# Optimization experiments

Hardware: AMD Instinct MI355X
Metric: run time of the kernel (lower is better)

Reference implementation:

```python
import jax, jax.numpy as jnp
import numpy as np

B, T, D, HS = 8, 2048, 768, 64  # batch, seq, n_embd, head_size


def setup_inputs() -> dict:
    key = jax.random.key(0)
    kx, kq, kk, kv = jax.random.split(key, 4)
    scale = 1.0 / np.sqrt(D)
    return {
        "x": jax.random.normal(kx, (B, T, D), dtype=jnp.float32),
        "Wq": jax.random.normal(kq, (D, HS), dtype=jnp.float32) * scale,
        "Wk": jax.random.normal(kk, (D, HS), dtype=jnp.float32) * scale,
        "Wv": jax.random.normal(kv, (D, HS), dtype=jnp.float32) * scale,
    }


def reference(x, Wq, Wk, Wv):
    # q,k,v: [B,T,HS]
    q = jnp.einsum("btd,dh->bth", x, Wq)
    k = jnp.einsum("btd,dh->bth", x, Wk)
    v = jnp.einsum("btd,dh->bth", x, Wv)
    hs = k.shape[-1]
    # scaled scores: [B,T,T]
    wei = jnp.einsum("bth,bsh->bts", q, k) * (hs ** -0.5)
    # causal mask (lower-triangular keeps, upper -> -inf)
    causal = jnp.tril(jnp.ones((x.shape[1], x.shape[1]), dtype=bool))
    wei = jnp.where(causal[None, :, :], wei, -jnp.inf)
    wei = jax.nn.softmax(wei, axis=-1)
    return jnp.einsum("bts,bsh->bth", wei, v)
```

## Files before the change

### kernel.cpp

```cpp
#include <hip/hip_runtime.h>

typedef float  f32x4  __attribute__((ext_vector_type(4)));
typedef short  short8 __attribute__((ext_vector_type(8)));
typedef short  short4_ __attribute__((ext_vector_type(4)));

constexpr int Bb = 8, T = 2048, D = 768, HS = 64;
constexpr int BT = Bb * T;
constexpr int QT = T / 64;
constexpr int PSTRIDE = 64 * 64 + 128;

__device__ __forceinline__ short f2bf(float f) {
    unsigned u = __builtin_bit_cast(unsigned, f);
    unsigned r = (u + 0x7FFFu + ((u >> 16) & 1u)) >> 16;
    return (short)r;
}

__device__ __forceinline__ void gld_lds16(const short* g, short* l) {
    __builtin_amdgcn_global_load_lds(
        (const __attribute__((address_space(1))) unsigned int*)g,
        (__attribute__((address_space(3))) unsigned int*)l, 16, 0, 0);
}

__global__ __launch_bounds__(256) void wt_kernel(const float* __restrict__ Wq,
                                                 const float* __restrict__ Wk,
                                                 const float* __restrict__ Wv,
                                                 short* __restrict__ Wt) {
    int n = blockIdx.x;
    const float* W = (n < 64) ? Wq : (n < 128) ? Wk : Wv;
    int c = n & 63;
    for (int kk = threadIdx.x; kk < D; kk += 256)
        Wt[n * D + kk] = f2bf(W[kk * HS + c]);
}

__global__ __launch_bounds__(512) void qkv_proj(const float* __restrict__ x,
                                                const short* __restrict__ Wt,
                                                short* __restrict__ qws,
                                                short* __restrict__ kws,
                                                short* __restrict__ vtg) {
    __shared__ alignas(16) short xs[2][64 * 72];
    __shared__ alignas(16) short wtile[2][192 * 64];

    const int tid  = threadIdx.x;
    const int lane = tid & 63, w = tid >> 6;
    const int lo   = lane & 15, hi = lane >> 4;
    const int wr   = w >> 2, wc = w & 3;
    const int row0 = blockIdx.x * 64;
    const int b    = row0 >> 11, t0 = row0 & 2047;

    const int xr0 = tid >> 4, xsg = tid & 15;
    const float* xsrc0 = &x[(size_t)(row0 + xr0) * D + xsg * 4];
    const float* xsrc1 = &x[(size_t)(row0 + 32 + xr0) * D + xsg * 4];

    f32x4 acc[6];
#pragma unroll
    for (int j = 0; j < 6; j++) acc[j] = f32x4{0.f, 0.f, 0.f, 0.f};

#define STAGE(bb, kc)                                                          \
    {                                                                          \
        _Pragma("unroll")                                                      \
        for (int it = 0; it < 3; it++) {                                       \
            int ci = it * 512 + w * 64 + lane;                                 \
            int n = ci >> 3, seg = ci & 7;                                     \
            gld_lds16(&Wt[(size_t)n * D + (kc) * 64 + ((seg ^ (n & 7)) << 3)], \
                      &wtile[bb][(it * 512 + w * 64) * 8]);                    \
        }                                                                      \
        float4 f0 = *reinterpret_cast<const float4*>(xsrc0 + (kc) * 64);       \
        float4 f1 = *reinterpret_cast<const float4*>(xsrc1 + (kc) * 64);       \
        short4_ h0, h1;                                                        \
        h0[0] = f2bf(f0.x); h0[1] = f2bf(f0.y); h0[2] = f2bf(f0.z); h0[3] = f2bf(f0.w); \
        h1[0] = f2bf(f1.x); h1[1] = f2bf(f1.y); h1[2] = f2bf(f1.z); h1[3] = f2bf(f1.w); \
        *reinterpret_cast<short4_*>(&xs[bb][xr0 * 72 + xsg * 4]) = h0;         \
        *reinterpret_cast<short4_*>(&xs[bb][(32 + xr0) * 72 + xsg * 4]) = h1;  \
    }

    STAGE(0, 0);
    __syncthreads();

    for (int kc = 0; kc < 12; kc++) {
        const int bb = kc & 1;
        if (kc + 1 < 12) STAGE(bb ^ 1, kc + 1);

#pragma unroll
        for (int m = 0; m < 2; m++) {
            const int ar = (wr * 32 + m * 16 + lo) * 72;
            short8 a0 = *reinterpret_cast<const short8*>(&xs[bb][ar + hi * 8]);
            short8 a1 = *reinterpret_cast<const short8*>(&xs[bb][ar + 32 + hi * 8]);
#pragma unroll
            for (int j = 0; j < 3; j++) {
                const int row = wc * 48 + j * 16 + lo;
                const int rx  = (row & 7) << 3;
                short8 b0 = *reinterpret_cast<const short8*>(
                    &wtile[bb][row * 64 + ((hi << 3) ^ rx)]);
                short8 b1 = *reinterpret_cast<const short8*>(
                    &wtile[bb][row * 64 + (((hi + 4) << 3) ^ rx)]);
                acc[m * 3 + j] = __builtin_amdgcn_mfma_f32_16x16x32_bf16(a0, b0, acc[m * 3 + j], 0, 0, 0);
                acc[m * 3 + j] = __builtin_amdgcn_mfma_f32_16x16x32_bf16(a1, b1, acc[m * 3 + j], 0, 0, 0);
            }
        }
        __syncthreads();
    }
#undef STAGE

#pragma unroll
    for (int m = 0; m < 2; m++) {
        const int orow = row0 + wr * 32 + m * 16 + hi * 4;
#pragma unroll
        for (int j = 0; j < 3; j++) {
            const int cb = wc * 48 + j * 16;
            const f32x4 a = acc[m * 3 + j];
            if (cb < 64) {
#pragma unroll
                for (int r = 0; r < 4; r++)
                    qws[(size_t)(orow + r) * HS + cb + lo] = f2bf(a[r] * 0.125f);
            } else if (cb < 128) {
#pragma unroll
                for (int r = 0; r < 4; r++)
                    kws[(size_t)(orow + r) * HS + cb - 64 + lo] = f2bf(a[r]);
            } else {
                short4_ pv;
#pragma unroll
                for (int r = 0; r < 4; r++) pv[r] = f2bf(a[r]);
                *reinterpret_cast<short4_*>(
                    &vtg[((size_t)b * 64 + cb - 128 + lo) * T + t0 + wr * 32 + m * 16 + hi * 4]) = pv;
            }
        }
    }
}

__global__ __launch_bounds__(256, 4) void attn(const short* __restrict__ qg,
                                               const short* __restrict__ kg,
                                               const short* __restrict__ vtg,
                                               float* __restrict__ part, int S) {
    __shared__ short ks[2][64 * 64];
    __shared__ short vts[2][64 * 64];
    __shared__ short ps[4][16 * 64];

    const int tid  = threadIdx.x;
    const int lane = tid & 63, w = tid >> 6;
    const int lo   = lane & 15, hi = lane >> 4;
    const int bid  = blockIdx.x;
    const int per_b = QT * S;
    const int b    = bid / per_b;
    const int r2   = bid % per_b;
    const int qt   = 31 - (r2 / S);
    const int c    = r2 % S;
    const int nkt  = qt + 1;
    const int base = nkt / S, rem = nkt % S;
    const int niter = base + (c < rem ? 1 : 0);
    const int kt0   = c * base + (c < rem ? c : rem);
    float* pout = part + (size_t)((b * QT + qt) * S + c) * PSTRIDE;

    float m_ = -1e30f, l_ = 0.0f;
    f32x4 oacc[4];
#pragma unroll
    for (int i = 0; i < 4; i++) oacc[i] = f32x4{0.f, 0.f, 0.f, 0.f};

    if (niter > 0) {
        const int qrow = qt * 64 + w * 16 + lo;
        const size_t qbase = ((size_t)b * T + qrow) * HS;
        short8 qa0 = *reinterpret_cast<const short8*>(&qg[qbase + hi * 8]);
        short8 qa1 = *reinterpret_cast<const short8*>(&qg[qbase + 32 + hi * 8]);

        const int srow = tid >> 2, scs = tid & 3, r7 = srow & 7;
        const int w0 = srow * 64 + (((scs * 2)     ^ r7) << 3);
        const int w1 = srow * 64 + (((scs * 2 + 1) ^ r7) << 3);
        const size_t kgoff = (size_t)b * T * HS;
        const size_t vgoff = ((size_t)b * 64 + srow) * T;

        short8 ka, kb2, va, vb;
        {
            const short* kp = &kg[kgoff + (size_t)(kt0 * 64 + srow) * HS + scs * 16];
            ka = *reinterpret_cast<const short8*>(kp);
            kb2 = *reinterpret_cast<const short8*>(kp + 8);
            const short* vp = &vtg[vgoff + kt0 * 64 + scs * 16];
            va = *reinterpret_cast<const short8*>(vp);
            vb = *reinterpret_cast<const short8*>(vp + 8);
        }
        *reinterpret_cast<short8*>(&ks[0][w0])  = ka;
        *reinterpret_cast<short8*>(&ks[0][w1])  = kb2;
        *reinterpret_cast<short8*>(&vts[0][w0]) = va;
        *reinterpret_cast<short8*>(&vts[0][w1]) = vb;

        const int pswz = (lo & 7) << 3;
        int cur = 0;
        for (int i = 0; i < niter; i++) {
            const int kt = kt0 + i;
            if (i + 1 < niter) {
                const short* kp = &kg[kgoff + (size_t)((kt + 1) * 64 + srow) * HS + scs * 16];
                ka = *reinterpret_cast<const short8*>(kp);
                kb2 = *reinterpret_cast<const short8*>(kp + 8);
                const short* vp = &vtg[vgoff + (kt + 1) * 64 + scs * 16];
                va = *reinterpret_cast<const short8*>(vp);
                vb = *reinterpret_cast<const short8*>(vp + 8);
            }
            __syncthreads();

            f32x4 sacc[4];
#pragma unroll
            for (int nt = 0; nt < 4; nt++) sacc[nt] = f32x4{0.f, 0.f, 0.f, 0.f};
            __builtin_amdgcn_s_setprio(1);
#pragma unroll
            for (int nt = 0; nt < 4; nt++) {
                const int row = nt * 16 + lo, rr = row & 7;
                short8 b0 = *reinterpret_cast<const short8*>(
                    &ks[cur][row * 64 + ((hi ^ rr) << 3)]);
                short8 b1 = *reinterpret_cast<const short8*>(
                    &ks[cur][row * 64 + (((hi + 4) ^ rr) << 3)]);
                sacc[nt] = __builtin_amdgcn_mfma_f32_16x16x32_bf16(b0, qa0, sacc[nt], 0, 0, 0);
                sacc[nt] = __builtin_amdgcn_mfma_f32_16x16x32_bf16(b1, qa1, sacc[nt], 0, 0, 0);
            }
            __builtin_amdgcn_s_setprio(0);

            if (kt == qt) {
#pragma unroll
                for (int nt = 0; nt < 4; nt++)
#pragma unroll
                    for (int r = 0; r < 4; r++)
                        if (nt * 16 + hi * 4 + r > w * 16 + lo) sacc[nt][r] = -1e30f;
            }

            float tm = fmaxf(fmaxf(fmaxf(sacc[0][0], sacc[0][1]), fmaxf(sacc[0][2], sacc[0][3])),
                             fmaxf(fmaxf(sacc[1][0], sacc[1][1]), fmaxf(sacc[1][2], sacc[1][3])));
            tm = fmaxf(tm, fmaxf(fmaxf(fmaxf(sacc[2][0], sacc[2][1]), fmaxf(sacc[2][2], sacc[2][3])),
                                 fmaxf(fmaxf(sacc[3][0], sacc[3][1]), fmaxf(sacc[3][2], sacc[3][3]))));
            tm = fmaxf(tm, __shfl_xor(tm, 16));
            tm = fmaxf(tm, __shfl_xor(tm, 32));

            if (!__all(tm <= m_ + 8.0f)) {
                float mnew = fmaxf(m_, tm);
                float corr = __expf(m_ - mnew);
                l_ *= corr;
#pragma unroll
                for (int r = 0; r < 4; r++) {
                    float cr = __shfl(corr, (lane & 48) | (hi * 4 + r));
#pragma unroll
                    for (int nt = 0; nt < 4; nt++) oacc[nt][r] *= cr;
                }
                m_ = mnew;
            }

#pragma unroll
            for (int nt = 0; nt < 4; nt++)
#pragma unroll
                for (int r = 0; r < 4; r++) {
                    float p = __expf(sacc[nt][r] - m_);
                    l_ += p;
                    const int key = nt * 16 + hi * 4 + r;
                    ps[w][lo * 64 + (key ^ pswz)] = f2bf(p);
                }

            short8 pa0 = *reinterpret_cast<const short8*>(
                &ps[w][lo * 64 + ((hi << 3) ^ pswz)]);
            short8 pa1 = *reinterpret_cast<const short8*>(
                &ps[w][lo * 64 + (((hi + 4) << 3) ^ pswz)]);
            __builtin_amdgcn_s_setprio(1);
#pragma unroll
            for (int nt = 0; nt < 4; nt++) {
                const int row = nt * 16 + lo, rr = row & 7;
                short8 b0 = *reinterpret_cast<const short8*>(
                    &vts[cur][row * 64 + ((hi ^ rr) << 3)]);
                short8 b1 = *reinterpret_cast<const short8*>(
                    &vts[cur][row * 64 + (((hi + 4) ^ rr) << 3)]);
                oacc[nt] = __builtin_amdgcn_mfma_f32_16x16x32_bf16(pa0, b0, oacc[nt], 0, 0, 0);
                oacc[nt] = __builtin_amdgcn_mfma_f32_16x16x32_bf16(pa1, b1, oacc[nt], 0, 0, 0);
            }
            __builtin_amdgcn_s_setprio(0);

            if (i + 1 < niter) {
                *reinterpret_cast<short8*>(&ks[cur ^ 1][w0])  = ka;
                *reinterpret_cast<short8*>(&ks[cur ^ 1][w1])  = kb2;
                *reinterpret_cast<short8*>(&vts[cur ^ 1][w0]) = va;
                *reinterpret_cast<short8*>(&vts[cur ^ 1][w1]) = vb;
            }
            cur ^= 1;
        }
    }

    float lt = l_;
    lt += __shfl_xor(lt, 16);
    lt += __shfl_xor(lt, 32);

#pragma unroll
    for (int nt = 0; nt < 4; nt++)
#pragma unroll
        for (int r = 0; r < 4; r++)
            pout[(w * 16 + hi * 4 + r) * 64 + nt * 16 + lo] = oacc[nt][r];
    float mfor[4], lfor[4];
#pragma unroll
    for (int r = 0; r < 4; r++) {
        mfor[r] = __shfl(m_, (lane & 48) | (hi * 4 + r));
        lfor[r] = __shfl(lt, (lane & 48) | (hi * 4 + r));
    }
    if (lo == 0) {
#pragma unroll
        for (int r = 0; r < 4; r++) {
            const int row = w * 16 + hi * 4 + r;
            pout[4096 + row] = mfor[r];
            pout[4160 + row] = lfor[r];
        }
    }
}

__global__ __launch_bounds__(256) void combine(const float* __restrict__ part,
                                               float* __restrict__ out, int S) {
    const int bid = blockIdx.x;
    const int b = bid >> 5, qt = bid & 31;
    const float* p = part + (size_t)bid * S * PSTRIDE;
    const int row = threadIdx.x >> 2, cs = threadIdx.x & 3;

    float mv[4], lv[4], av[4];
    float M = -1e30f;
    for (int s = 0; s < S; s++) {
        mv[s] = p[(size_t)s * PSTRIDE + 4096 + row];
        lv[s] = p[(size_t)s * PSTRIDE + 4160 + row];
        M = fmaxf(M, mv[s]);
    }
    float den = 0.0f;
    for (int s = 0; s < S; s++) { av[s] = __expf(mv[s] - M); den += lv[s] * av[s]; }
    float inv = 1.0f / den;

    float* o = out + ((size_t)b * T + qt * 64 + row) * HS + cs * 16;
#pragma unroll
    for (int i = 0; i < 4; i++) {
        float4 res = make_float4(0.f, 0.f, 0.f, 0.f);
        for (int s = 0; s < S; s++) {
            float4 v = *reinterpret_cast<const float4*>(
                p + (size_t)s * PSTRIDE + row * 64 + cs * 16 + i * 4);
            res.x += v.x * av[s]; res.y += v.y * av[s];
            res.z += v.z * av[s]; res.w += v.w * av[s];
        }
        res.x *= inv; res.y *= inv; res.z *= inv; res.w *= inv;
        *reinterpret_cast<float4*>(o + i * 4) = res;
    }
}

extern "C" void kernel_launch(void* const* d_in, const int* in_sizes, int n_in,
                              void* d_out, int out_size, void* d_ws, size_t ws_size,
                              hipStream_t stream) {
    const float* x  = (const float*)d_in[0];
    const float* Wq = (const float*)d_in[1];
    const float* Wk = (const float*)d_in[2];
    const float* Wv = (const float*)d_in[3];
    float* out = (float*)d_out;

    short* ws   = (short*)d_ws;
    short* qws  = ws;
    short* kws  = qws + (size_t)BT * HS;
    short* vtws = kws + (size_t)BT * HS;
    short* Wt   = vtws + (size_t)BT * HS;
    float* part = (float*)(Wt + (size_t)192 * D);

    const size_t fixed = (size_t)3 * BT * HS * 2 + (size_t)192 * D * 2;
    int S = 4;
    while (S > 1 && fixed + (size_t)Bb * QT * S * PSTRIDE * 4 > ws_size) S >>= 1;

    wt_kernel<<<192, 256, 0, stream>>>(Wq, Wk, Wv, Wt);
    qkv_proj<<<BT / 64, 512, 0, stream>>>(x, Wt, qws, kws, vtws);
    attn<<<Bb * QT * S, 256, 0, stream>>>(qws, kws, vtws, part, S);
    combine<<<Bb * QT, 256, 0, stream>>>(part, out, S);
}
```

Baseline: 56.24 us.

## Triple-buffer QKV projection with async global-to-LDS loads for x and W

The QKV projection kernel now loads the fp32 x tile straight into LDS with global_load_lds, using an XOR swizzle. The bf16 conversion moves to fragment-load time, after the LDS read. Both the x and W tiles are triple-buffered with three stages prefetched. Manual vmcnt waits plus raw s_barrier replace __syncthreads, so loads can stay in flight across iterations. This should hide global-load latency and take the register round-trip for x off the load path. In exchange, LDS use is much larger, which may cut occupancy, and each x element is converted redundantly by the waves that share it.

```diff
diff --git a/kernel.cpp b/kernel.cpp
--- a/kernel.cpp
+++ b/kernel.cpp
@@ -15,7 +15,7 @@
     return (short)r;
 }
 
-__device__ __forceinline__ void gld_lds16(const short* g, short* l) {
+__device__ __forceinline__ void gld_lds16(const void* g, void* l) {
     __builtin_amdgcn_global_load_lds(
         (const __attribute__((address_space(1))) unsigned int*)g,
         (__attribute__((address_space(3))) unsigned int*)l, 16, 0, 0);
@@ -37,8 +37,8 @@
                                                 short* __restrict__ qws,
                                                 short* __restrict__ kws,
                                                 short* __restrict__ vtg) {
-    __shared__ alignas(16) short xs[2][64 * 72];
-    __shared__ alignas(16) short wtile[2][192 * 64];
+    __shared__ alignas(16) short wtile[3][192 * 64];
+    __shared__ alignas(16) float xls[3][64 * 64];
 
     const int tid  = threadIdx.x;
     const int lane = tid & 63, w = tid >> 6;
@@ -47,59 +47,86 @@
     const int row0 = blockIdx.x * 64;
     const int b    = row0 >> 11, t0 = row0 & 2047;
 
-    const int xr0 = tid >> 4, xsg = tid & 15;
-    const float* xsrc0 = &x[(size_t)(row0 + xr0) * D + xsg * 4];
-    const float* xsrc1 = &x[(size_t)(row0 + 32 + xr0) * D + xsg * 4];
-
     f32x4 acc[6];
 #pragma unroll
     for (int j = 0; j < 6; j++) acc[j] = f32x4{0.f, 0.f, 0.f, 0.f};
 
-#define STAGE(bb, kc)                                                          \
+#define STAGE_W(bufi, kc)                                                      \
     {                                                                          \
         _Pragma("unroll")                                                      \
         for (int it = 0; it < 3; it++) {                                       \
             int ci = it * 512 + w * 64 + lane;                                 \
             int n = ci >> 3, seg = ci & 7;                                     \
             gld_lds16(&Wt[(size_t)n * D + (kc) * 64 + ((seg ^ (n & 7)) << 3)], \
-                      &wtile[bb][(it * 512 + w * 64) * 8]);                    \
+                      &wtile[bufi][(it * 512 + w * 64) * 8]);                  \
         }                                                                      \
-        float4 f0 = *reinterpret_cast<const float4*>(xsrc0 + (kc) * 64);       \
-        float4 f1 = *reinterpret_cast<const float4*>(xsrc1 + (kc) * 64);       \
-        short4_ h0, h1;                                                        \
-        h0[0] = f2bf(f0.x); h0[1] = f2bf(f0.y); h0[2] = f2bf(f0.z); h0[3] = f2bf(f0.w); \
-        h1[0] = f2bf(f1.x); h1[1] = f2bf(f1.y); h1[2] = f2bf(f1.z); h1[3] = f2bf(f1.w); \
-        *reinterpret_cast<short4_*>(&xs[bb][xr0 * 72 + xsg * 4]) = h0;         \
-        *reinterpret_cast<short4_*>(&xs[bb][(32 + xr0) * 72 + xsg * 4]) = h1;  \
-    }
-
-    STAGE(0, 0);
-    __syncthreads();
-
+    }
+#define STAGE_X(bufi, kc)                                                      \
+    {                                                                          \
+        _Pragma("unroll")                                                      \
+        for (int it = 0; it < 2; it++) {                                       \
+            int idx = it * 512 + tid;                                          \
+            int row = idx >> 4, g = idx & 15;                                  \
+            int sg = (g & 8) | ((g & 7) ^ (row & 7));                          \
+            gld_lds16(&x[(size_t)(row0 + row) * D + (kc) * 64 + sg * 4],       \
+                      &xls[bufi][(it * 512 + w * 64) * 4]);                    \
+        }                                                                      \
+    }
+
+    STAGE_W(0, 0); STAGE_X(0, 0);
+    STAGE_W(1, 1); STAGE_X(1, 1);
+    STAGE_W(2, 2); STAGE_X(2, 2);
+
+#pragma unroll
     for (int kc = 0; kc < 12; kc++) {
-        const int bb = kc & 1;
-        if (kc + 1 < 12) STAGE(bb ^ 1, kc + 1);
-
+        if (kc <= 9)       asm volatile("s_waitcnt vmcnt(10)" ::: "memory");
+        else if (kc == 10) asm volatile("s_waitcnt vmcnt(5)" ::: "memory");
+        else               asm volatile("s_waitcnt vmcnt(0)" ::: "memory");
+        __builtin_amdgcn_s_barrier();
+        __builtin_amdgcn_sched_barrier(0);
+
+        const int buf = kc % 3;
 #pragma unroll
         for (int m = 0; m < 2; m++) {
-            const int ar = (wr * 32 + m * 16 + lo) * 72;
-            short8 a0 = *reinterpret_cast<const short8*>(&xs[bb][ar + hi * 8]);
-            short8 a1 = *reinterpret_cast<const short8*>(&xs[bb][ar + 32 + hi * 8]);
+            const int row = wr * 32 + m * 16 + lo;
+            const int rg  = row & 7;
+            float4 f00 = *reinterpret_cast<const float4*>(
+                &xls[buf][row * 64 + (((2 * hi) ^ rg)) * 4]);
+            float4 f01 = *reinterpret_cast<const float4*>(
+                &xls[buf][row * 64 + (((2 * hi + 1) ^ rg)) * 4]);
+            float4 f10 = *reinterpret_cast<const float4*>(
+                &xls[buf][row * 64 + (8 + ((2 * hi) ^ rg)) * 4]);
+            float4 f11 = *reinterpret_cast<const float4*>(
+                &xls[buf][row * 64 + (8 + ((2 * hi + 1) ^ rg)) * 4]);
+            short8 a0, a1;
+#pragma unroll
+            for (int e = 0; e < 4; e++) {
+                a0[e]     = f2bf(f00[e]);
+                a0[e + 4] = f2bf(f01[e]);
+                a1[e]     = f2bf(f10[e]);
+                a1[e + 4] = f2bf(f11[e]);
+            }
 #pragma unroll
             for (int j = 0; j < 3; j++) {
-                const int row = wc * 48 + j * 16 + lo;
-                const int rx  = (row & 7) << 3;
+                const int brow = wc * 48 + j * 16 + lo;
+                const int rx   = (brow & 7) << 3;
                 short8 b0 = *reinterpret_cast<const short8*>(
-                    &wtile[bb][row * 64 + ((hi << 3) ^ rx)]);
+                    &wtile[buf][brow * 64 + ((hi << 3) ^ rx)]);
                 short8 b1 = *reinterpret_cast<const short8*>(
-                    &wtile[bb][row * 64 + (((hi + 4) << 3) ^ rx)]);
+                    &wtile[buf][brow * 64 + (((hi + 4) << 3) ^ rx)]);
                 acc[m * 3 + j] = __builtin_amdgcn_mfma_f32_16x16x32_bf16(a0, b0, acc[m * 3 + j], 0, 0, 0);
                 acc[m * 3 + j] = __builtin_amdgcn_mfma_f32_16x16x32_bf16(a1, b1, acc[m * 3 + j], 0, 0, 0);
             }
         }
-        __syncthreads();
-    }
-#undef STAGE
+        __builtin_amdgcn_sched_barrier(0);
+        __builtin_amdgcn_s_barrier();
+        if (kc <= 8) {
+            STAGE_W(buf, kc + 3);
+            STAGE_X(buf, kc + 3);
+        }
+    }
+#undef STAGE_W
+#undef STAGE_X
 
 #pragma unroll
     for (int m = 0; m < 2; m++) {
```

After: 54.81 us. 1.03x faster.
